# Optimization experiments

Measured on AMD Instinct MI355X. Metric: run time of the kernel, lower is better.

The kernel has to match this reference:

```python
import jax, jax.numpy as jnp
import numpy as np
import math

N_HEADS = 16
EMBD = 1024
D_HEAD = EMBD // N_HEADS


def setup_inputs() -> dict:
    key = jax.random.key(0)
    ks = jax.random.split(key, 5)
    s = 1.0 / math.sqrt(EMBD)
    return {
        "x": jax.random.normal(ks[0], (2, 2048, EMBD), dtype=jnp.float32),
        "w_in": jax.random.normal(ks[1], (EMBD, 3 * EMBD), dtype=jnp.float32) * s,
        "b_in": jax.random.normal(ks[2], (3 * EMBD,), dtype=jnp.float32) * 0.02,
        "w_out": jax.random.normal(ks[3], (EMBD, EMBD), dtype=jnp.float32) * s,
        "b_out": jax.random.normal(ks[4], (EMBD,), dtype=jnp.float32) * 0.02,
    }


def reference(x, w_in, b_in, w_out, b_out):
    # x: [B, S, D]
    B, S, D = x.shape
    qkv = x @ w_in + b_in                      # [B, S, 3D]
    q, k, v = jnp.split(qkv, 3, axis=-1)
    # [B, S, H, dh] -> [B, H, S, dh]
    def heads(t):
        return t.reshape(B, S, N_HEADS, D_HEAD).transpose(0, 2, 1, 3)
    q, k, v = heads(q), heads(k), heads(v)
    scores = jnp.einsum("bhqd,bhkd->bhqk", q, k)  # [B, H, S, S]
    # causal mask applied before scaling (as in original; -inf invariant to scale)
    causal = jnp.tril(jnp.ones((S, S), dtype=bool))
    scores = jnp.where(causal, scores, -jnp.inf)
    scores = scores / jnp.asarray(math.sqrt(D_HEAD), dtype=scores.dtype)
    attn = jax.nn.softmax(scores, axis=-1)
    out = jnp.einsum("bhqk,bhkd->bhqd", attn, v)  # [B, H, S, dh]
    out = out.transpose(0, 2, 1, 3).reshape(B, S, D)
    return out @ w_out + b_out
```

## Files before the change

kernel.cpp:

```cpp
#include <hip/hip_runtime.h>
#include <stdint.h>

#define DEVI __device__ __forceinline__

typedef __attribute__((ext_vector_type(8))) short short8;
typedef __attribute__((ext_vector_type(4))) float f32x4;
typedef __attribute__((ext_vector_type(4))) uint32_t u32x4;

DEVI unsigned short f2bf(float f) {
    union { float f; uint32_t u; } v; v.f = f;
    return (unsigned short)((v.u + 0x7FFFu + ((v.u >> 16) & 1u)) >> 16);
}

DEVI uint32_t cvtpk_bf16(float a, float b) {
    uint32_t r;
    asm("v_cvt_pk_bf16_f32 %0, %1, %2" : "=v"(r) : "v"(a), "v"(b));
    return r;
}

DEVI void perm32(uint32_t &a, uint32_t &b) {
    asm("v_permlane32_swap_b32 %0, %1" : "+v"(a), "+v"(b));
}
DEVI void perm16(uint32_t &a, uint32_t &b) {
    asm("v_permlane16_swap_b32 %0, %1" : "+v"(a), "+v"(b));
}

DEVI void gload16(const void* g, void* l) {
    __builtin_amdgcn_global_load_lds(
        (const __attribute__((address_space(1))) unsigned int*)g,
        (__attribute__((address_space(3))) unsigned int*)l, 16, 0, 0);
}

__global__ __launch_bounds__(256) void k_prep(
    const float* __restrict__ x, ushort* __restrict__ xb,
    const float* __restrict__ w_in, ushort* __restrict__ w_inT,
    const float* __restrict__ w_out, ushort* __restrict__ w_outT)
{
    const int bid = blockIdx.x;
    if (bid < 2048) {
        const int n4 = 4096 * 1024 / 4;
        int i = bid * 256 + threadIdx.x;
        const int stride = 2048 * 256;
        for (; i < n4; i += stride) {
            float4 v = ((const float4*)x)[i];
            ushort4 o;
            o.x = f2bf(v.x); o.y = f2bf(v.y); o.z = f2bf(v.z); o.w = f2bf(v.w);
            ((ushort4*)xb)[i] = o;
        }
        return;
    }
    const float* in; ushort* out; int R, C, t;
    if (bid < 5120) { in = w_in;  out = w_inT;  R = 1024; C = 3072; t = bid - 2048; }
    else            { in = w_out; out = w_outT; R = 1024; C = 1024; t = bid - 5120; }
    const int tpr = C / 32;
    const int c0 = (t % tpr) * 32, r0 = (t / tpr) * 32;
    __shared__ float tl[32][33];
    int lr = threadIdx.x >> 5, lc = threadIdx.x & 31;
    #pragma unroll
    for (int i = 0; i < 4; i++)
        tl[lr + 8*i][lc] = in[(size_t)(r0 + lr + 8*i)*C + c0 + lc];
    __syncthreads();
    #pragma unroll
    for (int i = 0; i < 4; i++)
        out[(size_t)(c0 + lr + 8*i)*R + r0 + lc] = f2bf(tl[lc][lr + 8*i]);
}

template<int MODE, int NJ>
__global__ __launch_bounds__(256, 2) void k_gemm(
    const ushort* __restrict__ A, const ushort* __restrict__ Bt,
    const float* __restrict__ bias,
    ushort* __restrict__ oQ, ushort* __restrict__ oK, ushort* __restrict__ oV,
    float* __restrict__ oF,
    int M, int N, int K, int S)
{
    __shared__ __align__(16) ushort As[128*64];
    __shared__ __align__(16) ushort Bs[NJ*32*64];
    const int tid = threadIdx.x;
    const int w = tid >> 6, l = tid & 63;

    int lin = blockIdx.y * gridDim.x + blockIdx.x;
    int nwg = gridDim.x * gridDim.y;
    int swz = (lin & 7) * (nwg >> 3) + (lin >> 3);
    const int m0 = (swz / gridDim.x) * 128, n0 = (swz % gridDim.x) * (NJ*32);

    const int wr = (w >> 1) * 64, wc = (w & 1) * (NJ*16);
    const int fr = l & 15, fg = l >> 4;
    const int lr8 = l >> 3;
    const int slot = (l & 7) ^ lr8;

    f32x4 acc[4][NJ] = {};

    const ushort* Abase = A + (size_t)(m0 + w*32 + lr8) * K + slot*8;
    const ushort* Bbase = Bt + (size_t)(n0 + w*(NJ*8) + lr8) * K + slot*8;

    for (int k0 = 0; k0 < K; k0 += 64) {
        __syncthreads();
        #pragma unroll
        for (int i = 0; i < 4; i++)
            gload16(Abase + (size_t)(8*i)*K + k0, &As[(w*32 + 8*i)*64]);
        #pragma unroll
        for (int i = 0; i < NJ; i++)
            gload16(Bbase + (size_t)(8*i)*K + k0, &Bs[(w*(NJ*8) + 8*i)*64]);
        __syncthreads();
        #pragma unroll
        for (int kk = 0; kk < 2; kk++) {
            short8 af[4], bfr[NJ];
            #pragma unroll
            for (int i = 0; i < 4; i++) {
                int ra = wr + i*16 + fr;
                af[i] = *(const short8*)((const char*)As + ra*128 + ((kk*64 + fg*16) ^ ((ra & 7) << 4)));
            }
            #pragma unroll
            for (int j = 0; j < NJ; j++) {
                int rb = wc + j*16 + fr;
                bfr[j] = *(const short8*)((const char*)Bs + rb*128 + ((kk*64 + fg*16) ^ ((rb & 7) << 4)));
            }
            #pragma unroll
            for (int i = 0; i < 4; i++)
                #pragma unroll
                for (int j = 0; j < NJ; j++)
                    acc[i][j] = __builtin_amdgcn_mfma_f32_16x16x32_bf16(af[i], bfr[j], acc[i][j], 0, 0, 0);
        }
    }

    if (MODE == 1) {
        #pragma unroll
        for (int j = 0; j < NJ; j++) {
            int n = n0 + wc + j*16 + fr;
            float bv = bias[n];
            #pragma unroll
            for (int i = 0; i < 4; i++) {
                int mrow = m0 + wr + i*16 + fg*4;
                #pragma unroll
                for (int r = 0; r < 4; r++)
                    oF[(size_t)(mrow + r)*N + n] = acc[i][j][r] + bv;
            }
        }
    } else {
        #pragma unroll
        for (int j = 0; j < NJ; j++) {
            int n = n0 + wc + j*16 + fr;
            int region = n >> 10;
            int h = (n & 1023) >> 6;
            int d = n & 63;
            float bv = bias[n];
            float scl = (region == 0) ? 0.18033688011112042f : 1.0f;
            #pragma unroll
            for (int i = 0; i < 4; i++) {
                int mrow = m0 + wr + i*16 + fg*4;
                int b = mrow >> 11;
                int s = mrow & 2047;
                if (region < 2) {
                    ushort* dst = (region == 0 ? oQ : oK) + ((size_t)(b*16 + h)*S)*64 + (size_t)d;
                    #pragma unroll
                    for (int r = 0; r < 4; r++)
                        dst[(size_t)(s + r)*64] = f2bf((acc[i][j][r] + bv) * scl);
                } else {
                    ushort* dst = oV + ((size_t)(b*16 + h)*64 + d)*S + s;
                    ushort4 pk;
                    pk.x = f2bf(acc[i][j][0] + bv);
                    pk.y = f2bf(acc[i][j][1] + bv);
                    pk.z = f2bf(acc[i][j][2] + bv);
                    pk.w = f2bf(acc[i][j][3] + bv);
                    *(ushort4*)dst = pk;
                }
            }
        }
    }
}

__global__ __launch_bounds__(128, 2) void k_attn(
    const ushort* __restrict__ Q,
    const ushort* __restrict__ Kb,
    const ushort* __restrict__ Vt,
    ushort* __restrict__ O,
    int S)
{
    __shared__ __align__(16) ushort Kt[2][64*64];
    __shared__ __align__(16) ushort Vs[2][64*64];

    const int tid = threadIdx.x, w = tid >> 6, l = tid & 63;
    const int bid = blockIdx.x;
    const int half = bid >> 9;
    const int r_ = bid & 511;
    const int h = r_ & 15, b = (r_ >> 4) & 1, p = r_ >> 5;
    const int qt = half ? p : (31 - p);
    const int bh = b * 16 + h;
    const int qw = qt * 64 + w * 32;
    const int fr = l & 15, fg = l >> 4;

    short8 qf[2][2];
    {
        const ushort* qp = Q + ((size_t)bh*S + qw + fr)*64 + fg*8;
        qf[0][0] = *(const short8*)(qp);
        qf[0][1] = *(const short8*)(qp + 32);
        qf[1][0] = *(const short8*)(qp + 16*64);
        qf[1][1] = *(const short8*)(qp + 16*64 + 32);
    }

    float l_[2] = {0.f, 0.f};
    f32x4 o_[2][4] = {};

    const int lr8 = l >> 3;
    const int slot = (l & 7) ^ lr8;
    const ushort* Ksrc = Kb + (size_t)bh*S*64;
    const ushort* Vsrc = Vt + (size_t)bh*64*S;

    const int nt = qt + 1;

    auto stage = [&](int buf, int j0) {
        #pragma unroll
        for (int i = 0; i < 4; i++) {
            int rb = w*32 + i*8;
            gload16(Ksrc + (size_t)(j0 + rb + lr8)*64 + slot*8, &Kt[buf][rb*64]);
            gload16(Vsrc + (size_t)(rb + lr8)*S + j0 + slot*8, &Vs[buf][rb*64]);
        }
    };

    stage(0, 0);
    __syncthreads();
    int cur = 0;

    for (int jt = 0; jt < nt; jt++) {
        const int j0 = jt * 64;
        if (jt + 1 < nt) stage(cur ^ 1, j0 + 64);

        f32x4 sa[2][4] = {};
        __builtin_amdgcn_s_setprio(1);
        #pragma unroll
        for (int kk = 0; kk < 2; kk++) {
            short8 kf[4];
            #pragma unroll
            for (int f = 0; f < 4; f++) {
                int row = f*16 + fr;
                kf[f] = *(const short8*)((const char*)Kt[cur] + row*128 + ((kk*64 + fg*16) ^ ((row & 7) << 4)));
            }
            #pragma unroll
            for (int t = 0; t < 2; t++)
                #pragma unroll
                for (int f = 0; f < 4; f++)
                    sa[t][f] = __builtin_amdgcn_mfma_f32_16x16x32_bf16(kf[f], qf[t][kk], sa[t][f], 0, 0, 0);
        }
        __builtin_amdgcn_s_setprio(0);

        if (jt == nt - 1) {
            #pragma unroll
            for (int t = 0; t < 2; t++) {
                int qg = qw + t*16 + fr;
                #pragma unroll
                for (int f = 0; f < 4; f++) {
                    int base = j0 + f*16 + fg*4 - qg;
                    #pragma unroll
                    for (int r = 0; r < 4; r++)
                        if (base + r > 0) sa[t][f][r] = -1e30f;
                }
            }
        }

        uint32_t cw[2][4][2];
        #pragma unroll
        for (int t = 0; t < 2; t++)
            #pragma unroll
            for (int f = 0; f < 4; f++) {
                float p0 = __builtin_amdgcn_exp2f(sa[t][f][0]);
                float p1 = __builtin_amdgcn_exp2f(sa[t][f][1]);
                float p2 = __builtin_amdgcn_exp2f(sa[t][f][2]);
                float p3 = __builtin_amdgcn_exp2f(sa[t][f][3]);
                l_[t] += (p0 + p1) + (p2 + p3);
                cw[t][f][0] = cvtpk_bf16(p0, p1);
                cw[t][f][1] = cvtpk_bf16(p2, p3);
            }

        __builtin_amdgcn_s_setprio(1);
        #pragma unroll
        for (int kk = 0; kk < 2; kk++) {
            short8 pf[2];
            #pragma unroll
            for (int t = 0; t < 2; t++) {
                uint32_t a0 = cw[t][2*kk][0], b0 = cw[t][2*kk + 1][0];
                perm32(a0, b0); perm16(a0, b0);
                uint32_t a1 = cw[t][2*kk][1], b1 = cw[t][2*kk + 1][1];
                perm32(a1, b1); perm16(a1, b1);
                u32x4 uw; uw[0] = a0; uw[1] = a1; uw[2] = b0; uw[3] = b1;
                pf[t] = __builtin_bit_cast(short8, uw);
            }
            #pragma unroll
            for (int f = 0; f < 4; f++) {
                int row = f*16 + fr;
                short8 vf = *(const short8*)((const char*)Vs[cur] + row*128 + ((kk*64 + fg*16) ^ ((row & 7) << 4)));
                #pragma unroll
                for (int t = 0; t < 2; t++)
                    o_[t][f] = __builtin_amdgcn_mfma_f32_16x16x32_bf16(vf, pf[t], o_[t][f], 0, 0, 0);
            }
        }
        __builtin_amdgcn_s_setprio(0);

        __syncthreads();
        cur ^= 1;
    }

    #pragma unroll
    for (int t = 0; t < 2; t++) {
        l_[t] += __shfl_xor(l_[t], 16);
        l_[t] += __shfl_xor(l_[t], 32);
    }

    #pragma unroll
    for (int t = 0; t < 2; t++) {
        float inv = 1.0f / l_[t];
        int qg = qw + t*16 + fr;
        #pragma unroll
        for (int f = 0; f < 4; f++) {
            ushort4 pk;
            pk.x = f2bf(o_[t][f][0] * inv);
            pk.y = f2bf(o_[t][f][1] * inv);
            pk.z = f2bf(o_[t][f][2] * inv);
            pk.w = f2bf(o_[t][f][3] * inv);
            *(ushort4*)&O[((size_t)(b*S + qg))*1024 + h*64 + f*16 + fg*4] = pk;
        }
    }
}

extern "C" void kernel_launch(void* const* d_in, const int* in_sizes, int n_in,
                              void* d_out, int out_size, void* d_ws, size_t ws_size,
                              hipStream_t stream)
{
    const float* x     = (const float*)d_in[0];
    const float* w_in  = (const float*)d_in[1];
    const float* b_in  = (const float*)d_in[2];
    const float* w_out = (const float*)d_in[3];
    const float* b_out = (const float*)d_in[4];
    float* out = (float*)d_out;

    const int B = 2, S = 2048, D = 1024, H = 16;
    const int M = B * S;

    if (ws_size < (40u << 20)) return;
    char* ws = (char*)d_ws;
    ushort* xb     = (ushort*)(ws);
    ushort* w_inT  = (ushort*)(ws + (8u << 20));
    ushort* w_outT = (ushort*)(ws + (14u << 20));
    ushort* qb     = (ushort*)(ws + (16u << 20));
    ushort* kb     = (ushort*)(ws + (24u << 20));
    ushort* vtb    = (ushort*)(ws + (32u << 20));

    k_prep<<<6144, 256, 0, stream>>>(x, xb, w_in, w_inT, w_out, w_outT);
    k_gemm<0,4><<<dim3(3*D/128, M/128), 256, 0, stream>>>(xb, w_inT, b_in, qb, kb, vtb, nullptr, M, 3*D, D, S);
    k_attn<<<1024, 128, 0, stream>>>(qb, kb, vtb, xb, S);
    k_gemm<1,2><<<dim3(D/64, M/128), 256, 0, stream>>>(xb, w_outT, b_out, nullptr, nullptr, nullptr, out, M, D, D, S);
}
```

Before: 102.4 us.

## Add 256x256-tile 8-wave ping-pong pipelined GEMM for QKV projection

Replaces the QKV projection GEMM with a new kernel that uses 256x256 output tiles, 512 threads and double-buffered LDS. Its phased schedule interleaves global-to-LDS loads of the next K-tile with MFMA work on the current one, using barriers and s_setprio to keep the matrix units busy. The aim is more data reuse per tile and latency hiding of global loads. In exchange the grid shrinks to 192 workgroups, fewer than the CU count, and the large LDS footprint limits occupancy. The old GEMM template is simplified to serve only the output projection.

```diff
diff --git a/kernel.cpp b/kernel.cpp
--- a/kernel.cpp
+++ b/kernel.cpp
@@ -65,13 +65,137 @@
         out[(size_t)(c0 + lr + 8*i)*R + r0 + lc] = f2bf(tl[lc][lr + 8*i]);
 }
 
+__global__ __launch_bounds__(512, 2) void k_gemm8(
+    const ushort* __restrict__ A, const ushort* __restrict__ Bt,
+    const float* __restrict__ bias,
+    ushort* __restrict__ oQ, ushort* __restrict__ oK, ushort* __restrict__ oV,
+    int M, int N, int K, int S)
+{
+    __shared__ __align__(16) ushort As[2][256*64];
+    __shared__ __align__(16) ushort Bs[2][256*64];
+    const int tid = threadIdx.x;
+    const int w = tid >> 6, l = tid & 63;
+    const int wm = w >> 2, wn = w & 3;
+
+    int lin = blockIdx.y * gridDim.x + blockIdx.x;
+    int nwg = gridDim.x * gridDim.y;
+    int swz = (lin & 7) * (nwg >> 3) + (lin >> 3);
+    const int m0 = (swz / gridDim.x) * 256, n0 = (swz % gridDim.x) * 256;
+
+    const int fr = l & 15, fg = l >> 4;
+    const int lr8 = l >> 3;
+    const int slot = (l & 7) ^ lr8;
+
+    const int NT = K >> 6;
+    f32x4 acc[8][4] = {};
+
+    const ushort* Ab = A + (size_t)(m0 + w*8 + lr8) * K + slot*8;
+    const ushort* Bb = Bt + (size_t)(n0 + w*8 + lr8) * K + slot*8;
+
+    auto stA = [&](int buf, int q, int kt) {
+        gload16(Ab + (size_t)(q*64) * K + kt*64, &As[buf][(q*64 + w*8) * 64]);
+    };
+    auto stB = [&](int buf, int q, int kt) {
+        gload16(Bb + (size_t)(q*64) * K + kt*64, &Bs[buf][(q*64 + w*8) * 64]);
+    };
+
+#define PHASE(BUF, IH, JH, STAGES) do {                                              \
+    short8 af[4][2], bf[2][2];                                                       \
+    _Pragma("unroll")                                                                \
+    for (int ii = 0; ii < 4; ii++) {                                                 \
+        int ra = wm*128 + ((IH)*4 + ii)*16 + fr;                                     \
+        _Pragma("unroll")                                                            \
+        for (int kk = 0; kk < 2; kk++)                                               \
+            af[ii][kk] = *(const short8*)((const char*)As[BUF] + ra*128 +            \
+                          ((kk*64 + fg*16) ^ ((ra & 7) << 4)));                      \
+    }                                                                                \
+    _Pragma("unroll")                                                                \
+    for (int jj = 0; jj < 2; jj++) {                                                 \
+        int rb = wn*64 + ((JH)*2 + jj)*16 + fr;                                      \
+        _Pragma("unroll")                                                            \
+        for (int kk = 0; kk < 2; kk++)                                               \
+            bf[jj][kk] = *(const short8*)((const char*)Bs[BUF] + rb*128 +            \
+                          ((kk*64 + fg*16) ^ ((rb & 7) << 4)));                      \
+    }                                                                                \
+    STAGES;                                                                          \
+    __builtin_amdgcn_s_barrier();                                                    \
+    asm volatile("s_waitcnt lgkmcnt(0)" ::: "memory");                               \
+    __builtin_amdgcn_s_setprio(1);                                                   \
+    _Pragma("unroll")                                                                \
+    for (int kk = 0; kk < 2; kk++)                                                   \
+        _Pragma("unroll")                                                            \
+        for (int ii = 0; ii < 4; ii++)                                               \
+            _Pragma("unroll")                                                        \
+            for (int jj = 0; jj < 2; jj++)                                           \
+                acc[(IH)*4 + ii][(JH)*2 + jj] = __builtin_amdgcn_mfma_f32_16x16x32_bf16( \
+                    af[ii][kk], bf[jj][kk], acc[(IH)*4 + ii][(JH)*2 + jj], 0, 0, 0); \
+    __builtin_amdgcn_s_setprio(0);                                                   \
+    __builtin_amdgcn_s_barrier();                                                    \
+} while (0)
+
+    stA(0, 0, 0); stA(0, 1, 0); stA(0, 2, 0); stA(0, 3, 0);
+    stB(0, 0, 0); stB(0, 1, 0); stB(0, 2, 0); stB(0, 3, 0);
+    stA(1, 0, 1); stA(1, 2, 1);
+
+    const int ND = NT >> 1;
+    for (int d = 0; d < ND; d++) {
+        const int kt1 = 2*d + 1;
+        const int kt2 = (2*d + 2 < NT) ? 2*d + 2 : 0;
+        const int kt3 = (2*d + 3 < NT) ? 2*d + 3 : 0;
+
+        asm volatile("s_waitcnt vmcnt(2)" ::: "memory");
+        PHASE(0, 0, 0, { stB(1, 0, kt1); stB(1, 1, kt1); });
+        PHASE(0, 0, 1, { stB(1, 2, kt1); stB(1, 3, kt1); });
+        PHASE(0, 1, 0, { stA(1, 1, kt1); stA(1, 3, kt1); });
+        PHASE(0, 1, 1, { stA(0, 0, kt2); stA(0, 2, kt2); });
+        asm volatile("s_waitcnt vmcnt(2)" ::: "memory");
+        PHASE(1, 0, 0, { stA(0, 1, kt2); stA(0, 3, kt2); });
+        PHASE(1, 0, 1, { stB(0, 0, kt2); stB(0, 1, kt2); });
+        PHASE(1, 1, 0, { stB(0, 2, kt2); stB(0, 3, kt2); });
+        PHASE(1, 1, 1, { stA(1, 0, kt3); stA(1, 2, kt3); });
+    }
+#undef PHASE
+
+    asm volatile("s_waitcnt vmcnt(0)" ::: "memory");
+
+    const int wr = wm*128, wc = wn*64;
+    #pragma unroll
+    for (int j = 0; j < 4; j++) {
+        int n = n0 + wc + j*16 + fr;
+        int region = n >> 10;
+        int h = (n & 1023) >> 6;
+        int d = n & 63;
+        float bv = bias[n];
+        float scl = (region == 0) ? 0.18033688011112042f : 1.0f;
+        #pragma unroll
+        for (int i = 0; i < 8; i++) {
+            int mrow = m0 + wr + i*16 + fg*4;
+            int b = mrow >> 11;
+            int s = mrow & 2047;
+            if (region < 2) {
+                ushort* dst = (region == 0 ? oQ : oK) + ((size_t)(b*16 + h)*S)*64 + (size_t)d;
+                #pragma unroll
+                for (int r = 0; r < 4; r++)
+                    dst[(size_t)(s + r)*64] = f2bf((acc[i][j][r] + bv) * scl);
+            } else {
+                ushort* dst = oV + ((size_t)(b*16 + h)*64 + d)*S + s;
+                ushort4 pk;
+                pk.x = f2bf(acc[i][j][0] + bv);
+                pk.y = f2bf(acc[i][j][1] + bv);
+                pk.z = f2bf(acc[i][j][2] + bv);
+                pk.w = f2bf(acc[i][j][3] + bv);
+                *(ushort4*)dst = pk;
+            }
+        }
+    }
+}
+
 template<int MODE, int NJ>
 __global__ __launch_bounds__(256, 2) void k_gemm(
     const ushort* __restrict__ A, const ushort* __restrict__ Bt,
     const float* __restrict__ bias,
-    ushort* __restrict__ oQ, ushort* __restrict__ oK, ushort* __restrict__ oV,
     float* __restrict__ oF,
-    int M, int N, int K, int S)
+    int M, int N, int K)
 {
     __shared__ __align__(16) ushort As[128*64];
     __shared__ __align__(16) ushort Bs[NJ*32*64];
@@ -123,48 +247,16 @@
         }
     }
 
-    if (MODE == 1) {
-        #pragma unroll
-        for (int j = 0; j < NJ; j++) {
-            int n = n0 + wc + j*16 + fr;
-            float bv = bias[n];
-            #pragma unroll
-            for (int i = 0; i < 4; i++) {
-                int mrow = m0 + wr + i*16 + fg*4;
-                #pragma unroll
-                for (int r = 0; r < 4; r++)
-                    oF[(size_t)(mrow + r)*N + n] = acc[i][j][r] + bv;
-            }
-        }
-    } else {
-        #pragma unroll
-        for (int j = 0; j < NJ; j++) {
-            int n = n0 + wc + j*16 + fr;
-            int region = n >> 10;
-            int h = (n & 1023) >> 6;
-            int d = n & 63;
-            float bv = bias[n];
-            float scl = (region == 0) ? 0.18033688011112042f : 1.0f;
-            #pragma unroll
-            for (int i = 0; i < 4; i++) {
-                int mrow = m0 + wr + i*16 + fg*4;
-                int b = mrow >> 11;
-                int s = mrow & 2047;
-                if (region < 2) {
-                    ushort* dst = (region == 0 ? oQ : oK) + ((size_t)(b*16 + h)*S)*64 + (size_t)d;
-                    #pragma unroll
-                    for (int r = 0; r < 4; r++)
-                        dst[(size_t)(s + r)*64] = f2bf((acc[i][j][r] + bv) * scl);
-                } else {
-                    ushort* dst = oV + ((size_t)(b*16 + h)*64 + d)*S + s;
-                    ushort4 pk;
-                    pk.x = f2bf(acc[i][j][0] + bv);
-                    pk.y = f2bf(acc[i][j][1] + bv);
-                    pk.z = f2bf(acc[i][j][2] + bv);
-                    pk.w = f2bf(acc[i][j][3] + bv);
-                    *(ushort4*)dst = pk;
-                }
-            }
+    #pragma unroll
+    for (int j = 0; j < NJ; j++) {
+        int n = n0 + wc + j*16 + fr;
+        float bv = bias[n];
+        #pragma unroll
+        for (int i = 0; i < 4; i++) {
+            int mrow = m0 + wr + i*16 + fg*4;
+            #pragma unroll
+            for (int r = 0; r < 4; r++)
+                oF[(size_t)(mrow + r)*N + n] = acc[i][j][r] + bv;
         }
     }
 }
@@ -345,7 +437,7 @@
     ushort* vtb    = (ushort*)(ws + (32u << 20));
 
     k_prep<<<6144, 256, 0, stream>>>(x, xb, w_in, w_inT, w_out, w_outT);
-    k_gemm<0,4><<<dim3(3*D/128, M/128), 256, 0, stream>>>(xb, w_inT, b_in, qb, kb, vtb, nullptr, M, 3*D, D, S);
+    k_gemm8<<<dim3(3*D/256, M/256), 512, 0, stream>>>(xb, w_inT, b_in, qb, kb, vtb, M, 3*D, D, S);
     k_attn<<<1024, 128, 0, stream>>>(qb, kb, vtb, xb, S);
-    k_gemm<1,2><<<dim3(D/64, M/128), 256, 0, stream>>>(xb, w_outT, b_out, nullptr, nullptr, nullptr, out, M, D, D, S);
-}
+    k_gemm<1,2><<<dim3(D/64, M/128), 256, 0, stream>>>(xb, w_outT, b_out, out, M, D, D);
+}
```

Result: slower. 113.1 us (+10.5%).

## Enlarge attention query tile to 128 rows per block to reuse K/V tiles

Applied to the files above, without the earlier changes.

Each attention block now handles 128 query rows instead of 64, with each wave covering 64 rows as two 32-row sub-tiles that share every staged 64-key K/V tile in shared memory. This halves the number of K/V tile loads per query and halves the grid to 512 blocks. Sub-tiles that lie entirely past the causal diagonal skip their compute, and the mask is applied only to sub-tiles that cross it. The cost is more accumulator and Q-fragment registers per thread, fewer blocks to spread across CUs, and some waves sitting idle at barriers on diagonal tiles.

```diff
diff --git a/kernel.cpp b/kernel.cpp
--- a/kernel.cpp
+++ b/kernel.cpp
@@ -181,32 +181,33 @@
 
     const int tid = threadIdx.x, w = tid >> 6, l = tid & 63;
     const int bid = blockIdx.x;
-    const int half = bid >> 9;
-    const int r_ = bid & 511;
+    const int half = bid >> 8;
+    const int r_ = bid & 255;
     const int h = r_ & 15, b = (r_ >> 4) & 1, p = r_ >> 5;
-    const int qt = half ? p : (31 - p);
+    const int qt = half ? p : (15 - p);
     const int bh = b * 16 + h;
-    const int qw = qt * 64 + w * 32;
+    const int qw = qt * 128 + w * 64;
     const int fr = l & 15, fg = l >> 4;
 
-    short8 qf[2][2];
+    short8 qf[4][2];
     {
         const ushort* qp = Q + ((size_t)bh*S + qw + fr)*64 + fg*8;
-        qf[0][0] = *(const short8*)(qp);
-        qf[0][1] = *(const short8*)(qp + 32);
-        qf[1][0] = *(const short8*)(qp + 16*64);
-        qf[1][1] = *(const short8*)(qp + 16*64 + 32);
-    }
-
-    float l_[2] = {0.f, 0.f};
-    f32x4 o_[2][4] = {};
+        #pragma unroll
+        for (int t = 0; t < 4; t++) {
+            qf[t][0] = *(const short8*)(qp + t*16*64);
+            qf[t][1] = *(const short8*)(qp + t*16*64 + 32);
+        }
+    }
+
+    float l_[4] = {0.f, 0.f, 0.f, 0.f};
+    f32x4 o_[4][4] = {};
 
     const int lr8 = l >> 3;
     const int slot = (l & 7) ^ lr8;
     const ushort* Ksrc = Kb + (size_t)bh*S*64;
     const ushort* Vsrc = Vt + (size_t)bh*64*S;
 
-    const int nt = qt + 1;
+    const int nt = 2*qt + 2;
 
     auto stage = [&](int buf, int j0) {
         #pragma unroll
@@ -221,92 +222,101 @@
     __syncthreads();
     int cur = 0;
 
+#define BODY(TP) do {                                                                     \
+    const int qbase = qw + (TP)*32;                                                       \
+    if (j0 < qbase + 32) {                     \
+        const bool domask = (j0 + 64 > qbase);                                            \
+        f32x4 sa[2][4] = {};                                                              \
+        __builtin_amdgcn_s_setprio(1);                                                    \
+        _Pragma("unroll")                                                                 \
+        for (int kk = 0; kk < 2; kk++) {                                                  \
+            short8 kf[4];                                                                 \
+            _Pragma("unroll")                                                             \
+            for (int f = 0; f < 4; f++) {                                                 \
+                int row = f*16 + fr;                                                      \
+                kf[f] = *(const short8*)((const char*)Kt[cur] + row*128 +                 \
+                         ((kk*64 + fg*16) ^ ((row & 7) << 4)));                           \
+            }                                                                             \
+            _Pragma("unroll")                                                             \
+            for (int t = 0; t < 2; t++)                                                   \
+                _Pragma("unroll")                                                         \
+                for (int f = 0; f < 4; f++)                                               \
+                    sa[t][f] = __builtin_amdgcn_mfma_f32_16x16x32_bf16(                   \
+                        kf[f], qf[(TP)*2 + t][kk], sa[t][f], 0, 0, 0);                    \
+        }                                                                                 \
+        __builtin_amdgcn_s_setprio(0);                                                    \
+        if (domask) {                                                                     \
+            _Pragma("unroll")                                                             \
+            for (int t = 0; t < 2; t++) {                                                 \
+                int qg = qbase + t*16 + fr;                                               \
+                _Pragma("unroll")                                                         \
+                for (int f = 0; f < 4; f++) {                                             \
+                    int base = j0 + f*16 + fg*4 - qg;                                     \
+                    _Pragma("unroll")                                                     \
+                    for (int r = 0; r < 4; r++)                                           \
+                        if (base + r > 0) sa[t][f][r] = -1e30f;                           \
+                }                                                                         \
+            }                                                                             \
+        }                                                                                 \
+        uint32_t cw[2][4][2];                                                             \
+        _Pragma("unroll")                                                                 \
+        for (int t = 0; t < 2; t++)                                                       \
+            _Pragma("unroll")                                                             \
+            for (int f = 0; f < 4; f++) {                                                 \
+                float p0 = __builtin_amdgcn_exp2f(sa[t][f][0]);                           \
+                float p1 = __builtin_amdgcn_exp2f(sa[t][f][1]);                           \
+                float p2 = __builtin_amdgcn_exp2f(sa[t][f][2]);                           \
+                float p3 = __builtin_amdgcn_exp2f(sa[t][f][3]);                           \
+                l_[(TP)*2 + t] += (p0 + p1) + (p2 + p3);                                  \
+                cw[t][f][0] = cvtpk_bf16(p0, p1);                                         \
+                cw[t][f][1] = cvtpk_bf16(p2, p3);                                         \
+            }                                                                             \
+        __builtin_amdgcn_s_setprio(1);                                                    \
+        _Pragma("unroll")                                                                 \
+        for (int kk = 0; kk < 2; kk++) {                                                  \
+            short8 pf[2];                                                                 \
+            _Pragma("unroll")                                                             \
+            for (int t = 0; t < 2; t++) {                                                 \
+                uint32_t a0 = cw[t][2*kk][0], b0 = cw[t][2*kk + 1][0];                    \
+                perm32(a0, b0); perm16(a0, b0);                                           \
+                uint32_t a1 = cw[t][2*kk][1], b1 = cw[t][2*kk + 1][1];                    \
+                perm32(a1, b1); perm16(a1, b1);                                           \
+                u32x4 uw; uw[0] = a0; uw[1] = a1; uw[2] = b0; uw[3] = b1;                 \
+                pf[t] = __builtin_bit_cast(short8, uw);                                   \
+            }                                                                             \
+            _Pragma("unroll")                                                             \
+            for (int f = 0; f < 4; f++) {                                                 \
+                int row = f*16 + fr;                                                      \
+                short8 vf = *(const short8*)((const char*)Vs[cur] + row*128 +             \
+                             ((kk*64 + fg*16) ^ ((row & 7) << 4)));                       \
+                _Pragma("unroll")                                                         \
+                for (int t = 0; t < 2; t++)                                               \
+                    o_[(TP)*2 + t][f] = __builtin_amdgcn_mfma_f32_16x16x32_bf16(          \
+                        vf, pf[t], o_[(TP)*2 + t][f], 0, 0, 0);                           \
+            }                                                                             \
+        }                                                                                 \
+        __builtin_amdgcn_s_setprio(0);                                                    \
+    }                                                                                     \
+} while (0)
+
     for (int jt = 0; jt < nt; jt++) {
         const int j0 = jt * 64;
         if (jt + 1 < nt) stage(cur ^ 1, j0 + 64);
-
-        f32x4 sa[2][4] = {};
-        __builtin_amdgcn_s_setprio(1);
-        #pragma unroll
-        for (int kk = 0; kk < 2; kk++) {
-            short8 kf[4];
-            #pragma unroll
-            for (int f = 0; f < 4; f++) {
-                int row = f*16 + fr;
-                kf[f] = *(const short8*)((const char*)Kt[cur] + row*128 + ((kk*64 + fg*16) ^ ((row & 7) << 4)));
-            }
-            #pragma unroll
-            for (int t = 0; t < 2; t++)
-                #pragma unroll
-                for (int f = 0; f < 4; f++)
-                    sa[t][f] = __builtin_amdgcn_mfma_f32_16x16x32_bf16(kf[f], qf[t][kk], sa[t][f], 0, 0, 0);
-        }
-        __builtin_amdgcn_s_setprio(0);
-
-        if (jt == nt - 1) {
-            #pragma unroll
-            for (int t = 0; t < 2; t++) {
-                int qg = qw + t*16 + fr;
-                #pragma unroll
-                for (int f = 0; f < 4; f++) {
-                    int base = j0 + f*16 + fg*4 - qg;
-                    #pragma unroll
-                    for (int r = 0; r < 4; r++)
-                        if (base + r > 0) sa[t][f][r] = -1e30f;
-                }
-            }
-        }
-
-        uint32_t cw[2][4][2];
-        #pragma unroll
-        for (int t = 0; t < 2; t++)
-            #pragma unroll
-            for (int f = 0; f < 4; f++) {
-                float p0 = __builtin_amdgcn_exp2f(sa[t][f][0]);
-                float p1 = __builtin_amdgcn_exp2f(sa[t][f][1]);
-                float p2 = __builtin_amdgcn_exp2f(sa[t][f][2]);
-                float p3 = __builtin_amdgcn_exp2f(sa[t][f][3]);
-                l_[t] += (p0 + p1) + (p2 + p3);
-                cw[t][f][0] = cvtpk_bf16(p0, p1);
-                cw[t][f][1] = cvtpk_bf16(p2, p3);
-            }
-
-        __builtin_amdgcn_s_setprio(1);
-        #pragma unroll
-        for (int kk = 0; kk < 2; kk++) {
-            short8 pf[2];
-            #pragma unroll
-            for (int t = 0; t < 2; t++) {
-                uint32_t a0 = cw[t][2*kk][0], b0 = cw[t][2*kk + 1][0];
-                perm32(a0, b0); perm16(a0, b0);
-                uint32_t a1 = cw[t][2*kk][1], b1 = cw[t][2*kk + 1][1];
-                perm32(a1, b1); perm16(a1, b1);
-                u32x4 uw; uw[0] = a0; uw[1] = a1; uw[2] = b0; uw[3] = b1;
-                pf[t] = __builtin_bit_cast(short8, uw);
-            }
-            #pragma unroll
-            for (int f = 0; f < 4; f++) {
-                int row = f*16 + fr;
-                short8 vf = *(const short8*)((const char*)Vs[cur] + row*128 + ((kk*64 + fg*16) ^ ((row & 7) << 4)));
-                #pragma unroll
-                for (int t = 0; t < 2; t++)
-                    o_[t][f] = __builtin_amdgcn_mfma_f32_16x16x32_bf16(vf, pf[t], o_[t][f], 0, 0, 0);
-            }
-        }
-        __builtin_amdgcn_s_setprio(0);
-
+        BODY(0);
+        BODY(1);
         __syncthreads();
         cur ^= 1;
     }
+#undef BODY
 
     #pragma unroll
-    for (int t = 0; t < 2; t++) {
+    for (int t = 0; t < 4; t++) {
         l_[t] += __shfl_xor(l_[t], 16);
         l_[t] += __shfl_xor(l_[t], 32);
     }
 
     #pragma unroll
-    for (int t = 0; t < 2; t++) {
+    for (int t = 0; t < 4; t++) {
         float inv = 1.0f / l_[t];
         int qg = qw + t*16 + fr;
         #pragma unroll
@@ -346,6 +356,6 @@
 
     k_prep<<<6144, 256, 0, stream>>>(x, xb, w_in, w_inT, w_out, w_outT);
     k_gemm<0,4><<<dim3(3*D/128, M/128), 256, 0, stream>>>(xb, w_inT, b_in, qb, kb, vtb, nullptr, M, 3*D, D, S);
-    k_attn<<<1024, 128, 0, stream>>>(qb, kb, vtb, xb, S);
+    k_attn<<<512, 128, 0, stream>>>(qb, kb, vtb, xb, S);
     k_gemm<1,2><<<dim3(D/64, M/128), 256, 0, stream>>>(xb, w_outT, b_out, nullptr, nullptr, nullptr, out, M, D, D, S);
 }
```

Result: slower. 120.9 us (+18.0%).
